# Optimization experiments

Measured on AMD Instinct MI355X. Metric: run time of the kernel, lower is better.

## Reference

```python
import jax, jax.numpy as jnp
import numpy as np


def _segment_sparsemax(x, batch, B):
    """Per-group sparsemax over a flat ragged tensor.

    x: [N] float values; batch: [N] sorted int group ids in [0, B).
    Groups are contiguous, so an in-group descending sort is a stable
    lexsort on (batch, -x); per-group cumsum is a global cumsum minus the
    cumsum value just before each group's start offset.
    """
    N = x.shape[0]
    num_nodes = jax.ops.segment_sum(jnp.ones(N, jnp.int32), batch, num_segments=B)  # [B]
    start = jnp.concatenate([jnp.zeros(1, jnp.int32), jnp.cumsum(num_nodes)[:-1]])  # [B]

    # shift by per-group max for numerical stability (as in torch forward)
    gmax = jax.ops.segment_max(x, batch, num_segments=B)
    xs = x - gmax[batch]

    # descending sort within each contiguous group
    order = jnp.lexsort((-xs, batch))
    sx = xs[order]  # [N], group-wise descending; group layout unchanged

    # per-group cumulative sum via global cumsum + start offsets
    cs = jnp.cumsum(sx)
    off = jnp.where(start > 0, cs[jnp.maximum(start - 1, 0)], jnp.zeros((), sx.dtype))  # [B]
    seg_cs = cs - off[batch] - 1.0  # input_cumsum - 1.0

    # rho = 1..n_g within each group
    rho = (jnp.arange(N, dtype=jnp.int32) - start[batch] + 1).astype(xs.dtype)

    support = rho * sx > seg_cs  # [N] bool
    supp_size = jax.ops.segment_sum(support.astype(jnp.int32), batch, num_segments=B)  # [B]

    idx = jnp.maximum(supp_size + start - 1, 0)  # [B]
    tau = seg_cs[idx] / supp_size.astype(xs.dtype)  # [B]

    return jnp.maximum(xs - tau[batch], 0.0)


def setup_inputs() -> dict:
    key = jax.random.key(0)
    k1, k2 = jax.random.split(key)
    N = 8_388_608
    B = 4096
    x = jax.random.normal(k1, (N,), dtype=jnp.float32)
    batch = jnp.sort(jax.random.randint(k2, (N,), 0, B)).astype(jnp.int64)
    return {"x": x, "batch": batch, "num_groups": B}


def reference(x, batch, num_groups):
    batch = batch.astype(jnp.int32)
    return _segment_sparsemax(x, batch, int(num_groups))
```

## Files before the change

kernel.cpp:

```cpp
#include <hip/hip_runtime.h>

#define BLK 256
#define QPT 3
#define CAPB (QPT * BLK * 4)
#define CCAP 320


__device__ __forceinline__ float wave_max(float v) {
#pragma unroll
  for (int o = 32; o; o >>= 1) v = fmaxf(v, __shfl_xor(v, o));
  return v;
}
__device__ __forceinline__ float wave_sum(float v) {
#pragma unroll
  for (int o = 32; o; o >>= 1) v += __shfl_xor(v, o);
  return v;
}
__device__ __forceinline__ int wave_sum_i(int v) {
#pragma unroll
  for (int o = 32; o; o >>= 1) v += __shfl_xor(v, o);
  return v;
}

__device__ __forceinline__ void block_sum_cnt(float& s, int& c, float* redf, int* redi, int tid) {
  s = wave_sum(s); c = wave_sum_i(c);
  __syncthreads();
  if ((tid & 63) == 0) { redf[tid >> 6] = s; redi[tid >> 6] = c; }
  __syncthreads();
  s = redf[0] + redf[1] + redf[2] + redf[3];
  c = redi[0] + redi[1] + redi[2] + redi[3];
}

__device__ __forceinline__ int wave_lower_bound(const int* __restrict__ batch, int N,
                                                int target, int lane) {
  int lo = 0, hi = N;
  while (hi > lo) {
    const long long span = hi - lo;
    const int m = lo + (int)((span * (long long)(lane + 1)) / 65);
    const int flag = (batch[m] < target) ? 1 : 0;
    const unsigned long long bal = __ballot(flag);
    const int c = __popcll(bal);
    int nlo = lo, nhi = hi;
    if (c > 0)  nlo = lo + (int)((span * (long long)c) / 65) + 1;
    if (c < 64) nhi = lo + (int)((span * (long long)(c + 1)) / 65);
    lo = nlo; hi = nhi;
  }
  return lo;
}


extern "C" __global__ void __launch_bounds__(BLK)
build_starts_bs(const int* __restrict__ batch, int* __restrict__ starts,
                const int* __restrict__ pB, int N) {
  const int B = *pB;
  const int lane = threadIdx.x & 63;
  const int w    = threadIdx.x >> 6;
  const int wpg  = gridDim.x * (BLK / 64);
  for (int t = blockIdx.x * (BLK / 64) + w; t <= B; t += wpg) {
    int v;
    if (t == 0) v = 0;
    else if (t >= B) v = N;
    else v = wave_lower_bound(batch, N, t, lane);
    if (lane == 0) starts[t] = v;
  }
}


extern "C" __global__ void __launch_bounds__(BLK)
sparsemax_groups(const float* __restrict__ x, const int* __restrict__ starts,
                 const int* __restrict__ pB, float* __restrict__ out, int N) {
  __shared__ float redf[4];
  __shared__ int   redi[4];
  __shared__ float cand[CCAP];
  __shared__ float sorted[64];
  __shared__ int   s_cnt;
  __shared__ float s_csum;
  __shared__ float s_tau;
  const int tid  = threadIdx.x;
  const int lane = tid & 63;
  const int w    = tid >> 6;
  const int B = *pB;

  for (int g = blockIdx.x; g < B; g += gridDim.x) {
    const int s = starts[g];
    const int e = starts[g + 1];
    const int n = e - s;
    if (n <= 0) continue;
    const int a0 = s & ~3;

    if (e - a0 <= CAPB) {
      float4 r[QPT];
      float lmax = -INFINITY;
#pragma unroll
      for (int j = 0; j < QPT; ++j) {
        const int idx = a0 + (j * BLK + tid) * 4;
        float4 v;
        if (idx >= s && idx + 4 <= e) {
          v = *(const float4*)(x + idx);
        } else {
          v = make_float4(-INFINITY, -INFINITY, -INFINITY, -INFINITY);
          if (idx < e) {
            if (idx + 4 <= N) {
              v = *(const float4*)(x + idx);
            } else {
              if (idx + 0 < N) v.x = x[idx + 0];
              if (idx + 1 < N) v.y = x[idx + 1];
              if (idx + 2 < N) v.z = x[idx + 2];
              if (idx + 3 < N) v.w = x[idx + 3];
            }
            if (idx + 0 < s || idx + 0 >= e) v.x = -INFINITY;
            if (idx + 1 < s || idx + 1 >= e) v.y = -INFINITY;
            if (idx + 2 < s || idx + 2 >= e) v.z = -INFINITY;
            if (idx + 3 < s || idx + 3 >= e) v.w = -INFINITY;
          }
        }
        r[j] = v;
        lmax = fmaxf(lmax, fmaxf(fmaxf(v.x, v.y), fmaxf(v.z, v.w)));
      }
      lmax = wave_max(lmax);
      if (lane == 0) redf[w] = lmax;
      if (tid == 0) { s_cnt = 0; s_csum = 0.0f; }
      __syncthreads();
      const float gmax = fmaxf(fmaxf(redf[0], redf[1]), fmaxf(redf[2], redf[3]));
      const float thr = gmax - 1.0f;

      int cm = 0; float wsum = 0.0f;
#pragma unroll
      for (int j = 0; j < QPT; ++j) {
        const float vv[4] = {r[j].x, r[j].y, r[j].z, r[j].w};
#pragma unroll
        for (int t = 0; t < 4; ++t)
          if (vv[t] > thr) { cm++; wsum += vv[t] - gmax; }
      }
      int pfx = cm;
#pragma unroll
      for (int o = 1; o < 64; o <<= 1) {
        const int t2 = __shfl_up(pfx, o);
        if (lane >= o) pfx += t2;
      }
      int base = 0;
      if (lane == 63 && pfx > 0) base = atomicAdd(&s_cnt, pfx);
      base = __shfl(base, 63);
      int off = base + pfx - cm;
      if (cm > 0) {
#pragma unroll
        for (int j = 0; j < QPT; ++j) {
          const float vv[4] = {r[j].x, r[j].y, r[j].z, r[j].w};
#pragma unroll
          for (int t = 0; t < 4; ++t)
            if (vv[t] > thr) { if (off < CCAP) cand[off] = vv[t]; off++; }
        }
      }
      wsum = wave_sum(wsum);
      if (lane == 0) atomicAdd(&s_csum, wsum);
      __syncthreads();
      const int c = s_cnt;

      if (c <= 64) {
        if (w == 0) {
          const float v = (lane < c) ? cand[lane] - gmax : 0.0f;
          int rank = 0;
          for (int q = 0; q < c; ++q) {
            const float t = cand[q] - gmax;
            rank += (t > v) || (t == v && q < lane);
          }
          if (lane < c) sorted[rank] = v;
          const float sv = (lane < c) ? sorted[lane] : 0.0f;
          float cs = sv;
#pragma unroll
          for (int o = 1; o < 64; o <<= 1) {
            const float t2 = __shfl_up(cs, o);
            if (lane >= o) cs += t2;
          }
          const int flag = (lane < c) && (sv * (float)(lane + 1) > cs - 1.0f);
          const unsigned long long bal2 = __ballot(flag);
          const int k = 63 - __clzll(bal2);
          const float csk = __shfl(cs, k);
          if (lane == 0) s_tau = (csk - 1.0f) / (float)(k + 1);
        }
      } else if (c <= CCAP) {
        if (w == 0) {
          float tau = (s_csum - 1.0f) / (float)c;
          int cnt = c;
          for (int it = 0; it < 64; ++it) {
            float s2 = 0.0f; int c2 = 0;
            for (int q = lane; q < c; q += 64) {
              const float vs = cand[q] - gmax;
              if (vs > tau) { s2 += vs; c2++; }
            }
            s2 = wave_sum(s2); c2 = wave_sum_i(c2);
            if (c2 == cnt || c2 == 0) break;
            tau = (s2 - 1.0f) / (float)c2; cnt = c2;
          }
          if (lane == 0) s_tau = tau;
        }
      } else {
        float tau = (s_csum - 1.0f) / (float)c;
        int cnt = c;
        for (int it = 0; it < 64; ++it) {
          float s2 = 0.0f; int c2 = 0;
#pragma unroll
          for (int j = 0; j < QPT; ++j) {
            const float vv[4] = {r[j].x, r[j].y, r[j].z, r[j].w};
#pragma unroll
            for (int t = 0; t < 4; ++t) {
              const float vs = vv[t] - gmax;
              if (vs > tau) { s2 += vs; c2++; }
            }
          }
          block_sum_cnt(s2, c2, redf, redi, tid);
          if (c2 == cnt || c2 == 0) break;
          tau = (s2 - 1.0f) / (float)c2; cnt = c2;
        }
        if (tid == 0) s_tau = tau;
      }
      __syncthreads();
      const float sub = s_tau + gmax;

#pragma unroll
      for (int j = 0; j < QPT; ++j) {
        const int idx = a0 + (j * BLK + tid) * 4;
        if (idx >= e) continue;
        if (idx >= s && idx + 4 <= e) {
          float4 o4;
          o4.x = fmaxf(r[j].x - sub, 0.0f);
          o4.y = fmaxf(r[j].y - sub, 0.0f);
          o4.z = fmaxf(r[j].z - sub, 0.0f);
          o4.w = fmaxf(r[j].w - sub, 0.0f);
          *(float4*)(out + idx) = o4;
        } else {
          const float vv[4] = {r[j].x, r[j].y, r[j].z, r[j].w};
#pragma unroll
          for (int t = 0; t < 4; ++t) {
            const int p2 = idx + t;
            if (p2 >= s && p2 < e) out[p2] = fmaxf(vv[t] - sub, 0.0f);
          }
        }
      }
    } else {
      float gmax = -INFINITY;
      for (int i = s + tid; i < e; i += BLK) gmax = fmaxf(gmax, x[i]);
      gmax = wave_max(gmax);
      if (lane == 0) redf[w] = gmax;
      __syncthreads();
      gmax = fmaxf(fmaxf(redf[0], redf[1]), fmaxf(redf[2], redf[3]));
      float bs = 0.0f; int bc = 0;
      for (int i = s + tid; i < e; i += BLK) {
        const float vs = x[i] - gmax;
        if (vs > -1.0f) { bs += vs; bc++; }
      }
      block_sum_cnt(bs, bc, redf, redi, tid);
      float tau = (bs - 1.0f) / (float)bc;
      int cntS = bc;
      for (int it = 0; it < 64; ++it) {
        float s2 = 0.0f; int c2 = 0;
        for (int i = s + tid; i < e; i += BLK) {
          const float vs = x[i] - gmax;
          if (vs > tau) { s2 += vs; c2++; }
        }
        block_sum_cnt(s2, c2, redf, redi, tid);
        if (c2 == cntS || c2 == 0) break;
        tau = (s2 - 1.0f) / (float)c2; cntS = c2;
      }
      const float sub = tau + gmax;
      for (int i = s + tid; i < e; i += BLK) out[i] = fmaxf(x[i] - sub, 0.0f);
    }
  }
}

extern "C" void kernel_launch(void* const* d_in, const int* in_sizes, int n_in,
                              void* d_out, int out_size, void* d_ws, size_t ws_size,
                              hipStream_t stream) {
  const float* x     = (const float*)d_in[0];
  const int*   batch = (const int*)d_in[1];
  const int*   pB    = (const int*)d_in[2];
  float*       out   = (float*)d_out;
  const int N = in_sizes[0];

  int* starts = (int*)d_ws;

  build_starts_bs<<<dim3(1025), dim3(BLK), 0, stream>>>(batch, starts, pB, N);
  sparsemax_groups<<<dim3(4096), dim3(BLK), 0, stream>>>(x, starts, pB, out, N);
}
```

Measured before the change: 114.1 us.

## Compute sparsemax tau redundantly per wave and compact candidates via ballot

Candidate compaction now uses per-element ballots with popcount offsets in place of a wave prefix scan and a shared partial-sum atomic. Every wave computes tau redundantly for the small-candidate paths (rank via shuffles, no shared reads), which removes the final block barrier and broadcast. Tau is now computed in unshifted space, dropping the per-element gmax subtraction, and the grid is halved to 2048 blocks. This adds more LDS atomics (up to 12 per wave) and redundant sort work in every wave, and changes the fixed-point start of the iterative paths.

```diff
diff --git a/kernel.cpp b/kernel.cpp
--- a/kernel.cpp
+++ b/kernel.cpp
@@ -69,12 +69,11 @@
 extern "C" __global__ void __launch_bounds__(BLK)
 sparsemax_groups(const float* __restrict__ x, const int* __restrict__ starts,
                  const int* __restrict__ pB, float* __restrict__ out, int N) {
+  __shared__ float cand[CCAP];
+  __shared__ float sorted[4][64];
   __shared__ float redf[4];
   __shared__ int   redi[4];
-  __shared__ float cand[CCAP];
-  __shared__ float sorted[64];
   __shared__ int   s_cnt;
-  __shared__ float s_csum;
   __shared__ float s_tau;
   const int tid  = threadIdx.x;
   const int lane = tid & 63;
@@ -119,103 +118,86 @@
       }
       lmax = wave_max(lmax);
       if (lane == 0) redf[w] = lmax;
-      if (tid == 0) { s_cnt = 0; s_csum = 0.0f; }
+      if (tid == 0) s_cnt = 0;
       __syncthreads();
       const float gmax = fmaxf(fmaxf(redf[0], redf[1]), fmaxf(redf[2], redf[3]));
       const float thr = gmax - 1.0f;
 
-      int cm = 0; float wsum = 0.0f;
 #pragma unroll
       for (int j = 0; j < QPT; ++j) {
         const float vv[4] = {r[j].x, r[j].y, r[j].z, r[j].w};
 #pragma unroll
-        for (int t = 0; t < 4; ++t)
-          if (vv[t] > thr) { cm++; wsum += vv[t] - gmax; }
-      }
-      int pfx = cm;
-#pragma unroll
-      for (int o = 1; o < 64; o <<= 1) {
-        const int t2 = __shfl_up(pfx, o);
-        if (lane >= o) pfx += t2;
-      }
-      int base = 0;
-      if (lane == 63 && pfx > 0) base = atomicAdd(&s_cnt, pfx);
-      base = __shfl(base, 63);
-      int off = base + pfx - cm;
-      if (cm > 0) {
-#pragma unroll
-        for (int j = 0; j < QPT; ++j) {
-          const float vv[4] = {r[j].x, r[j].y, r[j].z, r[j].w};
-#pragma unroll
-          for (int t = 0; t < 4; ++t)
-            if (vv[t] > thr) { if (off < CCAP) cand[off] = vv[t]; off++; }
-        }
-      }
-      wsum = wave_sum(wsum);
-      if (lane == 0) atomicAdd(&s_csum, wsum);
+        for (int t = 0; t < 4; ++t) {
+          const bool p = vv[t] > thr;
+          const unsigned long long bal = __ballot(p);
+          if (bal) {
+            int base = 0;
+            if (lane == 0) base = atomicAdd(&s_cnt, __popcll(bal));
+            base = __shfl(base, 0);
+            if (p) {
+              const int off = base + __popcll(bal & ((1ull << lane) - 1ull));
+              if (off < CCAP) cand[off] = vv[t];
+            }
+          }
+        }
+      }
       __syncthreads();
       const int c = s_cnt;
 
+      float tau;
       if (c <= 64) {
-        if (w == 0) {
-          const float v = (lane < c) ? cand[lane] - gmax : 0.0f;
-          int rank = 0;
-          for (int q = 0; q < c; ++q) {
-            const float t = cand[q] - gmax;
-            rank += (t > v) || (t == v && q < lane);
-          }
-          if (lane < c) sorted[rank] = v;
-          const float sv = (lane < c) ? sorted[lane] : 0.0f;
-          float cs = sv;
-#pragma unroll
-          for (int o = 1; o < 64; o <<= 1) {
-            const float t2 = __shfl_up(cs, o);
-            if (lane >= o) cs += t2;
-          }
-          const int flag = (lane < c) && (sv * (float)(lane + 1) > cs - 1.0f);
-          const unsigned long long bal2 = __ballot(flag);
-          const int k = 63 - __clzll(bal2);
-          const float csk = __shfl(cs, k);
-          if (lane == 0) s_tau = (csk - 1.0f) / (float)(k + 1);
-        }
+        const float v = (lane < c) ? cand[lane] : 0.0f;
+        int rank = 0;
+        for (int q = 0; q < c; ++q) {
+          const float t = __shfl(v, q);
+          rank += (t > v) || (t == v && q < lane);
+        }
+        if (lane < c) sorted[w][rank] = v;
+        const float sv = (lane < c) ? sorted[w][lane] : 0.0f;
+        float cs = sv;
+#pragma unroll
+        for (int o = 1; o < 64; o <<= 1) {
+          const float t2 = __shfl_up(cs, o);
+          if (lane >= o) cs += t2;
+        }
+        const int flag = (lane < c) && (sv * (float)(lane + 1) > cs - 1.0f);
+        const unsigned long long bal2 = __ballot(flag);
+        const int k = 63 - __clzll(bal2);
+        const float csk = __shfl(cs, k);
+        tau = (csk - 1.0f) / (float)(k + 1);
       } else if (c <= CCAP) {
-        if (w == 0) {
-          float tau = (s_csum - 1.0f) / (float)c;
-          int cnt = c;
-          for (int it = 0; it < 64; ++it) {
-            float s2 = 0.0f; int c2 = 0;
-            for (int q = lane; q < c; q += 64) {
-              const float vs = cand[q] - gmax;
-              if (vs > tau) { s2 += vs; c2++; }
-            }
-            s2 = wave_sum(s2); c2 = wave_sum_i(c2);
-            if (c2 == cnt || c2 == 0) break;
-            tau = (s2 - 1.0f) / (float)c2; cnt = c2;
-          }
-          if (lane == 0) s_tau = tau;
-        }
-      } else {
-        float tau = (s_csum - 1.0f) / (float)c;
-        int cnt = c;
+        tau = thr;
+        int cnt = -1;
         for (int it = 0; it < 64; ++it) {
           float s2 = 0.0f; int c2 = 0;
+          for (int q = lane; q < c; q += 64) {
+            const float vv = cand[q];
+            if (vv > tau) { s2 += vv; c2++; }
+          }
+          s2 = wave_sum(s2); c2 = wave_sum_i(c2);
+          if (c2 == cnt || c2 == 0) break;
+          tau = (s2 - 1.0f) / (float)c2; cnt = c2;
+        }
+      } else {
+        tau = thr;
+        int cnt = -1;
+        for (int it = 0; it < 64; ++it) {
+          float s2 = 0.0f; int c2 = 0;
 #pragma unroll
           for (int j = 0; j < QPT; ++j) {
             const float vv[4] = {r[j].x, r[j].y, r[j].z, r[j].w};
 #pragma unroll
-            for (int t = 0; t < 4; ++t) {
-              const float vs = vv[t] - gmax;
-              if (vs > tau) { s2 += vs; c2++; }
-            }
+            for (int t = 0; t < 4; ++t)
+              if (vv[t] > tau) { s2 += vv[t]; c2++; }
           }
           block_sum_cnt(s2, c2, redf, redi, tid);
           if (c2 == cnt || c2 == 0) break;
           tau = (s2 - 1.0f) / (float)c2; cnt = c2;
         }
         if (tid == 0) s_tau = tau;
-      }
-      __syncthreads();
-      const float sub = s_tau + gmax;
+        __syncthreads();
+        tau = s_tau;
+      }
 
 #pragma unroll
       for (int j = 0; j < QPT; ++j) {
@@ -223,17 +205,17 @@
         if (idx >= e) continue;
         if (idx >= s && idx + 4 <= e) {
           float4 o4;
-          o4.x = fmaxf(r[j].x - sub, 0.0f);
-          o4.y = fmaxf(r[j].y - sub, 0.0f);
-          o4.z = fmaxf(r[j].z - sub, 0.0f);
-          o4.w = fmaxf(r[j].w - sub, 0.0f);
+          o4.x = fmaxf(r[j].x - tau, 0.0f);
+          o4.y = fmaxf(r[j].y - tau, 0.0f);
+          o4.z = fmaxf(r[j].z - tau, 0.0f);
+          o4.w = fmaxf(r[j].w - tau, 0.0f);
           *(float4*)(out + idx) = o4;
         } else {
           const float vv[4] = {r[j].x, r[j].y, r[j].z, r[j].w};
 #pragma unroll
           for (int t = 0; t < 4; ++t) {
             const int p2 = idx + t;
-            if (p2 >= s && p2 < e) out[p2] = fmaxf(vv[t] - sub, 0.0f);
+            if (p2 >= s && p2 < e) out[p2] = fmaxf(vv[t] - tau, 0.0f);
           }
         }
       }
@@ -244,26 +226,19 @@
       if (lane == 0) redf[w] = gmax;
       __syncthreads();
       gmax = fmaxf(fmaxf(redf[0], redf[1]), fmaxf(redf[2], redf[3]));
-      float bs = 0.0f; int bc = 0;
-      for (int i = s + tid; i < e; i += BLK) {
-        const float vs = x[i] - gmax;
-        if (vs > -1.0f) { bs += vs; bc++; }
-      }
-      block_sum_cnt(bs, bc, redf, redi, tid);
-      float tau = (bs - 1.0f) / (float)bc;
-      int cntS = bc;
+      float tau = gmax - 1.0f;
+      int cnt = -1;
       for (int it = 0; it < 64; ++it) {
         float s2 = 0.0f; int c2 = 0;
         for (int i = s + tid; i < e; i += BLK) {
-          const float vs = x[i] - gmax;
+          const float vs = x[i];
           if (vs > tau) { s2 += vs; c2++; }
         }
         block_sum_cnt(s2, c2, redf, redi, tid);
-        if (c2 == cntS || c2 == 0) break;
-        tau = (s2 - 1.0f) / (float)c2; cntS = c2;
-      }
-      const float sub = tau + gmax;
-      for (int i = s + tid; i < e; i += BLK) out[i] = fmaxf(x[i] - sub, 0.0f);
+        if (c2 == cnt || c2 == 0) break;
+        tau = (s2 - 1.0f) / (float)c2; cnt = c2;
+      }
+      for (int i = s + tid; i < e; i += BLK) out[i] = fmaxf(x[i] - tau, 0.0f);
     }
   }
 }
@@ -280,5 +255,5 @@
   int* starts = (int*)d_ws;
 
   build_starts_bs<<<dim3(1025), dim3(BLK), 0, stream>>>(batch, starts, pB, N);
-  sparsemax_groups<<<dim3(4096), dim3(BLK), 0, stream>>>(x, starts, pB, out, N);
-}
+  sparsemax_groups<<<dim3(2048), dim3(BLK), 0, stream>>>(x, starts, pB, out, N);
+}
```

New measurement: 115.4 us. Within noise of the previous version (+1.2%).
